# Optimization experiments

Measured on AMD Instinct MI355X. Metric: run time of the kernel, lower is better.

The kernel has to match this reference:

```python
import jax, jax.numpy as jnp
import numpy as np

N, R, D = 2048, 4, 256
TEMPERATURE = 1.0
CLAMP_MIN = 1e-8


def setup_inputs() -> dict:
    key = jax.random.key(0)
    a = jax.random.normal(key, (N, R, D), dtype=jnp.float32)
    return {"a": a}


def reference(a):
    n, r, d = a.shape
    # Full pairwise Gram tensor over (input i, context j) x (input k, context l)
    sim = jnp.einsum('ijd,kld->ikjl', a, a) / TEMPERATURE          # [N,N,r,r]
    # detached row-max over l for stability (matches sim.detach().max(-1, keepdim=True))
    sim_max = jax.lax.stop_gradient(jnp.max(sim, axis=-1, keepdims=True))
    dp = jnp.exp(sim - sim_max)                                    # [N,N,r,r]

    # Positive pairs: i == k, j != l
    diag = jnp.einsum('iijl->ijl', dp)                             # [N,r,r]
    offdiag_jl = ~jnp.eye(r, dtype=bool)                           # [r,r]
    sim_pos = jnp.sum(diag * offdiag_jl, axis=(1, 2)) / (r * (r - 1))  # [N]

    # Negative pairs: i != k, all (j,l); square then clamp, then per-i mean
    sq = jnp.maximum(jnp.square(dp), CLAMP_MIN)                    # [N,N,r,r]
    diag_sq = jnp.sum(jnp.maximum(jnp.square(diag), CLAMP_MIN), axis=(1, 2))  # [N]
    sim_neg = (jnp.sum(sq, axis=(1, 2, 3)) - diag_sq) / ((n - 1) * r * r)     # [N]

    lora_loss = -2.0 * sim_pos + sim_neg                           # [N]
    return jnp.mean(lora_loss)                                     # 'mean' reduction -> scalar
```

## Files before the change

### kernel.cpp

```cpp
#include <hip/hip_runtime.h>


#define PD   8192
#define KB   256
#define BM   128
#define BK   32
#define NIT  (KB / BK)

typedef __bf16 bf16x8 __attribute__((ext_vector_type(8)));
typedef float f32x4 __attribute__((ext_vector_type(4)));

__device__ __forceinline__ void gload16(const void* g, void* l) {
    __builtin_amdgcn_global_load_lds(
        (const __attribute__((address_space(1))) unsigned int*)g,
        (__attribute__((address_space(3))) unsigned int*)l, 16, 0, 0);
}

__device__ __forceinline__ int swz(int row) { return ((row >> 1) & 3) << 4; }

__device__ __forceinline__ float quadmax(float x) {
    int v = __builtin_amdgcn_mov_dpp(__builtin_bit_cast(int, x), 0xB1, 0xF, 0xF, true);
    float m = fmaxf(x, __builtin_bit_cast(float, v));
    v = __builtin_amdgcn_mov_dpp(__builtin_bit_cast(int, m), 0x4E, 0xF, 0xF, true);
    return fmaxf(m, __builtin_bit_cast(float, v));
}

__global__ __launch_bounds__(256)
void cvt_bf16(const float* __restrict__ A, __bf16* __restrict__ W) {
    const int idx = blockIdx.x * 256 + threadIdx.x;
    const float4 v0 = reinterpret_cast<const float4*>(A)[idx * 2];
    const float4 v1 = reinterpret_cast<const float4*>(A)[idx * 2 + 1];
    bf16x8 h;
    h[0] = (__bf16)v0.x; h[1] = (__bf16)v0.y; h[2] = (__bf16)v0.z; h[3] = (__bf16)v0.w;
    h[4] = (__bf16)v1.x; h[5] = (__bf16)v1.y; h[6] = (__bf16)v1.z; h[7] = (__bf16)v1.w;
    *reinterpret_cast<bf16x8*>(W + (size_t)idx * 8) = h;
}

__global__ __launch_bounds__(256)
void evd_mfma(const __bf16* __restrict__ W, float* __restrict__ out)
{
    __shared__ __bf16 lds[2][2][BM * BK];
    __shared__ float wsum[4];

    const int x = blockIdx.x, y = blockIdx.y;
    int bi, bk;
    if (x < 64 - y) { bi = y;      bk = y + x; }
    else            { bi = 63 - y; bk = x - 1; }

    const int tid = threadIdx.x;
    const int lane = tid & 63, wid = tid >> 6;
    const int wr = wid >> 1, wc = wid & 1;
    const int row0 = bi * BM, col0 = bk * BM;

    const int r0 = tid >> 2;
    const int r1 = 64 + r0;
    const int x0 = (tid & 3) * 16;
    const int ga0 = r0 * (KB * 2) + (x0 ^ swz(r0));
    const int ga1 = r1 * (KB * 2) + (x0 ^ swz(r1));
    const char* gAb = (const char*)(W + (size_t)row0 * KB);
    const char* gBb = (const char*)(W + (size_t)col0 * KB);
    const int ldsOff0 = wid * 1024;
    const int ldsOff1 = 4096 + wid * 1024;

    const int fr = lane & 15, kq = lane >> 4;
    int aOff[4], bOff[4];
#pragma unroll
    for (int m = 0; m < 4; ++m) {
        const int ra = wr * 64 + m * 16 + fr;
        const int rb = wc * 64 + m * 16 + fr;
        aOff[m] = ra * 64 + ((kq * 16) ^ swz(ra));
        bOff[m] = rb * 64 + ((kq * 16) ^ swz(rb));
    }

    f32x4 acc[4][4];
#pragma unroll
    for (int m = 0; m < 4; ++m)
#pragma unroll
        for (int n = 0; n < 4; ++n)
#pragma unroll
            for (int q = 0; q < 4; ++q) acc[m][n][q] = 0.f;

    {
        char* dA = (char*)&lds[0][0][0];
        char* dB = (char*)&lds[0][1][0];
        gload16(gAb + ga0, dA + ldsOff0);
        gload16(gAb + ga1, dA + ldsOff1);
        gload16(gBb + ga0, dB + ldsOff0);
        gload16(gBb + ga1, dB + ldsOff1);
    }

#pragma unroll
    for (int t = 0; t < NIT; ++t) {
        __syncthreads();
        if (t < NIT - 1) {
            const int kbyte = (t + 1) * (BK * 2);
            char* dA = (char*)&lds[(t + 1) & 1][0][0];
            char* dB = (char*)&lds[(t + 1) & 1][1][0];
            gload16(gAb + ga0 + kbyte, dA + ldsOff0);
            gload16(gAb + ga1 + kbyte, dA + ldsOff1);
            gload16(gBb + ga0 + kbyte, dB + ldsOff0);
            gload16(gBb + ga1 + kbyte, dB + ldsOff1);
        }
        const char* baseA = (const char*)&lds[t & 1][0][0];
        const char* baseB = (const char*)&lds[t & 1][1][0];
        bf16x8 af[4], bfr[4];
#pragma unroll
        for (int m = 0; m < 4; ++m) {
            af[m]  = *(const bf16x8*)(baseA + aOff[m]);
            bfr[m] = *(const bf16x8*)(baseB + bOff[m]);
        }
#pragma unroll
        for (int m = 0; m < 4; ++m)
#pragma unroll
            for (int n = 0; n < 4; ++n)
                acc[m][n] = __builtin_amdgcn_mfma_f32_16x16x32_bf16(af[m], bfr[n], acc[m][n], 0, 0, 0);
    }

    const float C_NEG = 1.0f / (2048.0f * 2047.0f * 16.0f);
    const float C_POS = 2.0f / (2048.0f * 12.0f);
    const bool diag = (bi == bk);
    const bool ik = ((lane >> 4) == ((lane & 15) >> 2));
    float nsum = 0.f, psum = 0.f;

#pragma unroll
    for (int m = 0; m < 4; ++m) {
#pragma unroll
        for (int n = 0; n < 4; ++n) {
            const bool dfrag = diag && (wr == wc) && (m == n);
#pragma unroll
            for (int r = 0; r < 4; ++r) {
                const float s = acc[m][n][r];
                const float mm = quadmax(s);
                const float d = s - mm;
                if (dfrag) {
                    const float dp = __expf(d);
                    if (ik) {
                        if (r != (lane & 3)) psum += dp;
                    } else {
                        nsum += fmaxf(dp * dp, 1e-8f);
                    }
                } else {
                    nsum += fmaxf(__expf(d + d), 1e-8f);
                }
            }
            if (!diag) {
                const float mm2 = fmaxf(fmaxf(acc[m][n][0], acc[m][n][1]),
                                        fmaxf(acc[m][n][2], acc[m][n][3]));
#pragma unroll
                for (int r = 0; r < 4; ++r) {
                    const float d = acc[m][n][r] - mm2;
                    nsum += fmaxf(__expf(d + d), 1e-8f);
                }
            }
        }
    }

    float contrib = C_NEG * nsum - C_POS * psum;

#pragma unroll
    for (int off = 32; off; off >>= 1) contrib += __shfl_down(contrib, off);
    if ((tid & 63) == 0) wsum[tid >> 6] = contrib;
    __syncthreads();
    if (tid == 0) atomicAdd(out, wsum[0] + wsum[1] + wsum[2] + wsum[3]);
}

extern "C" void kernel_launch(void* const* d_in, const int* in_sizes, int n_in,
                              void* d_out, int out_size, void* d_ws, size_t ws_size,
                              hipStream_t stream) {
    const float* A = (const float*)d_in[0];
    float* out = (float*)d_out;
    __bf16* W = (__bf16*)d_ws;
    hipMemsetAsync(out, 0, sizeof(float), stream);
    cvt_bf16<<<(PD * KB / 8) / 256, 256, 0, stream>>>(A, W);
    dim3 grid(65, 32);
    evd_mfma<<<grid, 256, 0, stream>>>(W, out);
}
```

Baseline: 102.6 us.

## Prefetch two stages ahead, fold exp scale into exp2, drop memset launch

The K-loop now issues global-to-LDS loads two stages ahead, using explicit vmcnt waits and raw barriers in place of __syncthreads, so load latency overlaps more MFMA work. The epilogue pre-scales accumulators by 2*log2(e) and calls the hardware exp2 directly, which removes a multiply and an add per exponential. The hipMemsetAsync that zeroed the output is removed and the zeroing moves into the conversion kernel, saving one launch. The hand-written waitcnt and barrier sequence is fragile if the compiler reorders or counts loads differently from what it assumes.

```diff
diff --git a/kernel.cpp b/kernel.cpp
--- a/kernel.cpp
+++ b/kernel.cpp
@@ -26,8 +26,10 @@
 }
 
 __global__ __launch_bounds__(256)
-void cvt_bf16(const float* __restrict__ A, __bf16* __restrict__ W) {
+void cvt_bf16(const float* __restrict__ A, __bf16* __restrict__ W,
+              float* __restrict__ out) {
     const int idx = blockIdx.x * 256 + threadIdx.x;
+    if (idx == 0) *out = 0.f;
     const float4 v0 = reinterpret_cast<const float4*>(A)[idx * 2];
     const float4 v1 = reinterpret_cast<const float4*>(A)[idx * 2 + 1];
     bf16x8 h;
@@ -80,27 +82,25 @@
 #pragma unroll
             for (int q = 0; q < 4; ++q) acc[m][n][q] = 0.f;
 
-    {
-        char* dA = (char*)&lds[0][0][0];
-        char* dB = (char*)&lds[0][1][0];
-        gload16(gAb + ga0, dA + ldsOff0);
-        gload16(gAb + ga1, dA + ldsOff1);
-        gload16(gBb + ga0, dB + ldsOff0);
-        gload16(gBb + ga1, dB + ldsOff1);
-    }
+    auto stage = [&](int t, int b) {
+        const int kbyte = t * (BK * 2);
+        char* dA = (char*)&lds[b][0][0];
+        char* dB = (char*)&lds[b][1][0];
+        gload16(gAb + ga0 + kbyte, dA + ldsOff0);
+        gload16(gAb + ga1 + kbyte, dA + ldsOff1);
+        gload16(gBb + ga0 + kbyte, dB + ldsOff0);
+        gload16(gBb + ga1 + kbyte, dB + ldsOff1);
+    };
+
+    stage(0, 0);
+    stage(1, 1);
 
 #pragma unroll
     for (int t = 0; t < NIT; ++t) {
-        __syncthreads();
-        if (t < NIT - 1) {
-            const int kbyte = (t + 1) * (BK * 2);
-            char* dA = (char*)&lds[(t + 1) & 1][0][0];
-            char* dB = (char*)&lds[(t + 1) & 1][1][0];
-            gload16(gAb + ga0 + kbyte, dA + ldsOff0);
-            gload16(gAb + ga1 + kbyte, dA + ldsOff1);
-            gload16(gBb + ga0 + kbyte, dB + ldsOff0);
-            gload16(gBb + ga1 + kbyte, dB + ldsOff1);
-        }
+        if (t == NIT - 1) asm volatile("s_waitcnt vmcnt(0)" ::: "memory");
+        else              asm volatile("s_waitcnt vmcnt(4)" ::: "memory");
+        __builtin_amdgcn_s_barrier();
+
         const char* baseA = (const char*)&lds[t & 1][0][0];
         const char* baseB = (const char*)&lds[t & 1][1][0];
         bf16x8 af[4], bfr[4];
@@ -108,6 +108,11 @@
         for (int m = 0; m < 4; ++m) {
             af[m]  = *(const bf16x8*)(baseA + aOff[m]);
             bfr[m] = *(const bf16x8*)(baseB + bOff[m]);
+        }
+        if (t + 2 < NIT) {
+            asm volatile("s_waitcnt lgkmcnt(0)" ::: "memory");
+            __builtin_amdgcn_s_barrier();
+            stage(t + 2, t & 1);
         }
 #pragma unroll
         for (int m = 0; m < 4; ++m)
@@ -118,6 +123,7 @@
 
     const float C_NEG = 1.0f / (2048.0f * 2047.0f * 16.0f);
     const float C_POS = 2.0f / (2048.0f * 12.0f);
+    const float SCL = 2.0f * 1.4426950408889634f;
     const bool diag = (bi == bk);
     const bool ik = ((lane >> 4) == ((lane & 15) >> 2));
     float nsum = 0.f, psum = 0.f;
@@ -126,31 +132,29 @@
     for (int m = 0; m < 4; ++m) {
 #pragma unroll
         for (int n = 0; n < 4; ++n) {
+            float yv[4];
+#pragma unroll
+            for (int q = 0; q < 4; ++q) yv[q] = SCL * acc[m][n][q];
             const bool dfrag = diag && (wr == wc) && (m == n);
 #pragma unroll
             for (int r = 0; r < 4; ++r) {
-                const float s = acc[m][n][r];
-                const float mm = quadmax(s);
-                const float d = s - mm;
+                const float d2 = yv[r] - quadmax(yv[r]);
                 if (dfrag) {
-                    const float dp = __expf(d);
+                    const float dp = __builtin_amdgcn_exp2f(0.5f * d2);
                     if (ik) {
                         if (r != (lane & 3)) psum += dp;
                     } else {
                         nsum += fmaxf(dp * dp, 1e-8f);
                     }
                 } else {
-                    nsum += fmaxf(__expf(d + d), 1e-8f);
+                    nsum += fmaxf(__builtin_amdgcn_exp2f(d2), 1e-8f);
                 }
             }
             if (!diag) {
-                const float mm2 = fmaxf(fmaxf(acc[m][n][0], acc[m][n][1]),
-                                        fmaxf(acc[m][n][2], acc[m][n][3]));
+                const float ymax = fmaxf(fmaxf(fmaxf(yv[0], yv[1]), yv[2]), yv[3]);
 #pragma unroll
-                for (int r = 0; r < 4; ++r) {
-                    const float d = acc[m][n][r] - mm2;
-                    nsum += fmaxf(__expf(d + d), 1e-8f);
-                }
+                for (int r = 0; r < 4; ++r)
+                    nsum += fmaxf(__builtin_amdgcn_exp2f(yv[r] - ymax), 1e-8f);
             }
         }
     }
@@ -170,8 +174,7 @@
     const float* A = (const float*)d_in[0];
     float* out = (float*)d_out;
     __bf16* W = (__bf16*)d_ws;
-    hipMemsetAsync(out, 0, sizeof(float), stream);
-    cvt_bf16<<<(PD * KB / 8) / 256, 256, 0, stream>>>(A, W);
+    cvt_bf16<<<(PD * KB / 8) / 256, 256, 0, stream>>>(A, W, out);
     dim3 grid(65, 32);
     evd_mfma<<<grid, 256, 0, stream>>>(W, out);
 }
```

New measurement: 98.96 us. -3.6%, faster.
